# Optimization experiments

Hardware: AMD Instinct MI355X
Metric: run time of the kernel (lower is better)

## Reference

```python
import jax, jax.numpy as jnp
import numpy as np

T, B, D = 200, 1024, 128
T_OBS = 140
L = 20       # rec_dims: encoder latent per mean/std
LAT = 32     # latents: generative latent dim
GRU_U = 200  # gru_units
UNITS = 100  # hidden units of ODE-func / z0 nets


def _lin(key, fan_in, fan_out):
    return jax.random.normal(key, (fan_in, fan_out), jnp.float32) / jnp.sqrt(jnp.float32(fan_in))


def setup_inputs() -> dict:
    key = jax.random.key(0)
    ks = jax.random.split(key, 20)
    gin = 2 * L + 2 * D  # GRU input: (mean,std) + (data,mask)
    inp = {
        "truth": jax.random.normal(ks[0], (T, B, D), jnp.float32),
        "t": jnp.arange(T, dtype=jnp.float32),
        "obs_idx": jnp.sort(jax.random.randint(ks[1], (T_OBS,), 0, T)),
        "eps": jax.random.normal(ks[2], (B, LAT), jnp.float32),
        # encoder ODE func (rec_layers=1 hidden layer of UNITS)
        "enc_w1": _lin(ks[3], L, UNITS), "enc_b1": jnp.zeros(UNITS, jnp.float32),
        "enc_w2": _lin(ks[4], UNITS, L), "enc_b2": jnp.zeros(L, jnp.float32),
        # GRU unit: update / reset / new-state nets
        "gru_uw1": _lin(ks[5], gin, GRU_U), "gru_ub1": jnp.zeros(GRU_U, jnp.float32),
        "gru_uw2": _lin(ks[6], GRU_U, 2 * L), "gru_ub2": jnp.zeros(2 * L, jnp.float32),
        "gru_rw1": _lin(ks[7], gin, GRU_U), "gru_rb1": jnp.zeros(GRU_U, jnp.float32),
        "gru_rw2": _lin(ks[8], GRU_U, 2 * L), "gru_rb2": jnp.zeros(2 * L, jnp.float32),
        "gru_nw1": _lin(ks[9], gin, GRU_U), "gru_nb1": jnp.zeros(GRU_U, jnp.float32),
        "gru_nw2": _lin(ks[10], GRU_U, 2 * L), "gru_nb2": jnp.zeros(2 * L, jnp.float32),
        # transform hidden -> z0 (mean,std)
        "z0_w1": _lin(ks[11], 2 * L, UNITS), "z0_b1": jnp.zeros(UNITS, jnp.float32),
        "z0_w2": _lin(ks[12], UNITS, 2 * LAT), "z0_b2": jnp.zeros(2 * LAT, jnp.float32),
        # decoder ODE func (gen_layers=2 hidden layers of UNITS)
        "dec_w1": _lin(ks[13], LAT, UNITS), "dec_b1": jnp.zeros(UNITS, jnp.float32),
        "dec_w2": _lin(ks[14], UNITS, UNITS), "dec_b2": jnp.zeros(UNITS, jnp.float32),
        "dec_w3": _lin(ks[15], UNITS, LAT), "dec_b3": jnp.zeros(LAT, jnp.float32),
        # readout latent -> data space
        "out_w": _lin(ks[16], LAT, D), "out_b": jnp.zeros(D, jnp.float32),
    }
    return inp


def _rk4(f, y, dt):
    k1 = f(y)
    k2 = f(y + 0.5 * dt * k1)
    k3 = f(y + 0.5 * dt * k2)
    k4 = f(y + dt * k3)
    return y + (dt / 6.0) * (k1 + 2.0 * k2 + 2.0 * k3 + k4)


def reference(truth, t, obs_idx, eps,
              enc_w1, enc_b1, enc_w2, enc_b2,
              gru_uw1, gru_ub1, gru_uw2, gru_ub2,
              gru_rw1, gru_rb1, gru_rw2, gru_rb2,
              gru_nw1, gru_nb1, gru_nw2, gru_nb2,
              z0_w1, z0_b1, z0_w2, z0_b2,
              dec_w1, dec_b1, dec_w2, dec_b2, dec_w3, dec_b3,
              out_w, out_b):
    enc_f = lambda y: jnp.tanh(y @ enc_w1 + enc_b1) @ enc_w2 + enc_b2
    dec_f = lambda z: (jnp.tanh(jnp.tanh(z @ dec_w1 + dec_b1) @ dec_w2 + dec_b2)
                       @ dec_w3 + dec_b3)

    # ----- ODE-RNN encoder, run_backwards=True over observed timesteps -----
    x_obs = truth[obs_idx][::-1]                     # [To, B, D], time-reversed
    t_obs = t[obs_idx][::-1]
    dts = jnp.concatenate([jnp.zeros(1, t.dtype), jnp.diff(t_obs)])  # <=0 steps

    def enc_step(carry, inp):
        ym, ys = carry                               # [B,L] each
        x, dt = inp
        ym = _rk4(enc_f, ym, dt)                     # evolve mean between obs
        xm = jnp.concatenate([x, jnp.ones_like(x)], -1)   # data + mask(=1)
        y = jnp.concatenate([ym, ys], -1)            # [B, 2L]
        yc = jnp.concatenate([y, xm], -1)            # [B, 2L+2D]
        u = jax.nn.sigmoid(jnp.tanh(yc @ gru_uw1 + gru_ub1) @ gru_uw2 + gru_ub2)
        r = jax.nn.sigmoid(jnp.tanh(yc @ gru_rw1 + gru_rb1) @ gru_rw2 + gru_rb2)
        nc = jnp.concatenate([y * r, xm], -1)
        ns = jnp.tanh(nc @ gru_nw1 + gru_nb1) @ gru_nw2 + gru_nb2
        nm, nsd = ns[:, :L], jnp.abs(ns[:, L:])
        new_y = (1.0 - u) * jnp.concatenate([nm, nsd], -1) + u * y
        return (new_y[:, :L], new_y[:, L:]), None

    nb = truth.shape[1]
    init = (jnp.zeros((nb, L), truth.dtype), jnp.zeros((nb, L), truth.dtype))
    (ym, ys), _ = jax.lax.scan(enc_step, init, (x_obs, dts))

    # ----- z0 posterior and sample (n_traj_samples=1) -----
    h = jnp.tanh(jnp.concatenate([ym, ys], -1) @ z0_w1 + z0_b1) @ z0_w2 + z0_b2
    z0_mean, z0_std = h[:, :LAT], jnp.abs(h[:, LAT:])
    z = z0_mean + eps * z0_std                       # [B, LAT]

    # ----- Neural ODE decoder over time_steps_to_predict = t -----
    def dec_step(zc, dt):
        zn = _rk4(dec_f, zc, dt)
        return zn, zn
    _, zs = jax.lax.scan(dec_step, z, jnp.diff(t))
    sol = jnp.concatenate([z[None], zs], 0)          # [T, B, LAT]

    out = sol @ out_w + out_b                        # [T, B, D]
    return jnp.transpose(out, (1, 0, 2))[None]       # [1, B, T, D]
```

## Files before the change

kernel.cpp:

```cpp
#include <hip/hip_runtime.h>
#include <math.h>

#define BB 1024
#define DD 128
#define NWG 256
#define CH 28
#define NCH 5

#define WS_WPACK 0
#define WS_B1E   81920
#define WS_W1Y   82560
#define WS_Y     106560
#define WS_Z     147520
#define WS_HPRE  180288
#define WS_SOL   180288

__device__ __forceinline__ float bcast(float v, int lane) {
    return __uint_as_float(__builtin_amdgcn_readlane(__float_as_uint(v), lane));
}

__device__ __forceinline__ float tanh_fast(float x) {
    const float t = __builtin_amdgcn_exp2f(x * 2.88539008177793f);
    return 1.f - 2.f * __builtin_amdgcn_rcpf(t + 1.f);
}

__global__ __launch_bounds__(256) void prep_kernel(
    const float* __restrict__ uw1, const float* __restrict__ ub1,
    const float* __restrict__ rw1, const float* __restrict__ rb1,
    const float* __restrict__ nw1, const float* __restrict__ nb1,
    float* __restrict__ ws)
{
    int tid = blockIdx.x * blockDim.x + threadIdx.x;
    int nth = gridDim.x * blockDim.x;
    for (int idx = tid; idx < 128 * 640; idx += nth) {
        int k = idx / 640, j = idx - k * 640;
        float v = 0.f;
        if (j < 600) {
            int g = j / 200, jj = j - g * 200;
            const float* w1 = (g == 0) ? uw1 : (g == 1) ? rw1 : nw1;
            v = w1[(40 + k) * 200 + jj];
        }
        ws[WS_WPACK + idx] = v;
    }
    for (int j = tid; j < 640; j += nth) {
        float s = 0.f;
        if (j < 600) {
            int g = j / 200, jj = j - g * 200;
            const float* w1 = (g == 0) ? uw1 : (g == 1) ? rw1 : nw1;
            const float* b1 = (g == 0) ? ub1 : (g == 1) ? rb1 : nb1;
            s = b1[jj];
            for (int k = 168; k < 296; ++k) s += w1[k * 200 + jj];
        }
        ws[WS_B1E + j] = s;
    }
    for (int idx = tid; idx < 40 * 600; idx += nth) {
        int k = idx / 600, j = idx - k * 600;
        int g = j / 200, jj = j - g * 200;
        const float* w1 = (g == 0) ? uw1 : (g == 1) ? rw1 : nw1;
        ws[WS_W1Y + idx] = w1[k * 200 + jj];
    }
}

__global__ __launch_bounds__(256) void hpre_gemm(
    const float* __restrict__ truth, const int* __restrict__ obs_idx,
    const float* __restrict__ ws, float* __restrict__ hpre, int s0)
{
    __shared__ float sx[64][68];
    __shared__ float sw[64][132];
    const int t0 = threadIdx.x;
    const int jt = blockIdx.x % 5;
    const int bt = (blockIdx.x / 5) % 16;
    const int sl = blockIdx.x / 80;
    const int oi = obs_idx[139 - (s0 + sl)];
    const int b0 = bt * 64;
    const float* wpack = ws + WS_WPACK;
    const float* b1e   = ws + WS_B1E;

    const int jj  = t0 & 15;
    const int bb4 = t0 >> 4;
    float acc[8][4];
#pragma unroll
    for (int m = 0; m < 8; ++m)
#pragma unroll
        for (int q = 0; q < 4; ++q) acc[m][q] = 0.f;

    for (int kh = 0; kh < 2; ++kh) {
        __syncthreads();
        for (int i = t0; i < 64 * 16; i += 256) {
            int bb = i >> 4, kq = i & 15;
            const float4 v = *(const float4*)&truth[((size_t)oi * BB + b0 + bb) * DD + kh * 64 + kq * 4];
            *(float4*)&sx[bb][kq * 4] = v;
        }
        for (int i = t0; i < 64 * 32; i += 256) {
            int kk = i >> 5, jq = i & 31;
            const float4 v = *(const float4*)&wpack[(kh * 64 + kk) * 640 + jt * 128 + jq * 4];
            *(float4*)&sw[kk][jq * 4] = v;
        }
        __syncthreads();
#pragma unroll 4
        for (int k = 0; k < 64; ++k) {
            float xv[4], wv[8];
#pragma unroll
            for (int q = 0; q < 4; ++q) xv[q] = sx[bb4 * 4 + q][k];
#pragma unroll
            for (int m = 0; m < 8; ++m) wv[m] = sw[k][jj + 16 * m];
#pragma unroll
            for (int m = 0; m < 8; ++m)
#pragma unroll
                for (int q = 0; q < 4; ++q) acc[m][q] += wv[m] * xv[q];
        }
    }
    const int bblk = bt * 16 + bb4;
#pragma unroll
    for (int m = 0; m < 8; ++m) {
        int j = jt * 128 + jj + 16 * m;
        if (j < 600) {
            float be = b1e[j];
#pragma unroll
            for (int q = 0; q < 4; ++q)
                hpre[(size_t)((sl * 256 + bblk) * 4 + q) * 600 + j] = acc[m][q] + be;
        }
    }
}

__global__ __launch_bounds__(256, 1) void enc_chunk(
    const float* __restrict__ tg, const int* __restrict__ obs_idx,
    const float* __restrict__ eps,
    const float* __restrict__ ew1, const float* __restrict__ eb1,
    const float* __restrict__ ew2, const float* __restrict__ eb2,
    const float* __restrict__ uw2, const float* __restrict__ ub2,
    const float* __restrict__ rw2, const float* __restrict__ rb2,
    const float* __restrict__ nw2, const float* __restrict__ nb2,
    const float* __restrict__ z0w1, const float* __restrict__ z0b1,
    const float* __restrict__ z0w2, const float* __restrict__ z0b2,
    float* __restrict__ ws, int s0)
{
    __shared__ float s_t[200];
    __shared__ int   s_oi[140];
    __shared__ __align__(16) float s_y[40][4];
    __shared__ __align__(16) float s_ytmp[20][4];
    __shared__ float s_kacc[20][4];
    __shared__ __align__(16) float s_hid[4][104];
    __shared__ float s_pe[20][4][2];
    __shared__ __align__(16) float s_ew1t[100 * 20];
    __shared__ __align__(16) float s_w2n[40 * 212];
    __shared__ __align__(16) float s_hur[4][416];
    __shared__ __align__(16) float s_hn[4][208];
    __shared__ float s_pw[80][4][4];
    __shared__ float s_pn[40][4][4];
    __shared__ float s_u[40][4];
    __shared__ __align__(16) float s_yr[40][4];
    __shared__ float s_z0o[4][64];

    const int t0 = threadIdx.x;
    const int bblk = blockIdx.x;
    const int b0 = bblk * 4;
    const float* hpre = ws + WS_HPRE;

    float rgy[3][40];
    float rew2h[52];
    float rw2q[2][52];
    float eb1_r = 0.f, eb2_r = 0.f, bur_r = 0.f, bn_r = 0.f;

    if (t0 < 200) {
#pragma unroll
        for (int g = 0; g < 3; ++g)
#pragma unroll
            for (int k = 0; k < 40; ++k)
                rgy[g][k] = ws[WS_W1Y + k * 600 + g * 200 + t0];
    }
    if (t0 < 100) eb1_r = eb1[t0];
    if (t0 < 160) {
        const int c2 = t0 % 20, kh = t0 / 80;
#pragma unroll
        for (int i = 0; i < 52; ++i) {
            const int row = kh * 52 + i;
            rew2h[i] = (row < 100) ? ew2[row * 20 + c2] : 0.f;
        }
    }
    if (t0 < 80) eb2_r = eb2[t0 % 20];
    if (t0 < 160) {
        const int p = t0 % 20, g = (t0 / 20) % 2, kq = t0 / 40;
        const float* w2 = g ? rw2 : uw2;
#pragma unroll
        for (int j = 0; j < 2; ++j)
#pragma unroll
            for (int i = 0; i < 52; ++i) {
                const int row = kq * 52 + i;
                rw2q[j][i] = (row < 200) ? w2[row * 40 + p + 20 * j] : 0.f;
            }
        bur_r = ((t0 % 80) < 40) ? ub2[t0 % 80] : rb2[(t0 % 80) - 40];
        bn_r = nb2[t0 % 40];
    }

    for (int i = t0; i < 2000; i += 256) { int k = i / 100, c = i % 100; s_ew1t[c * 20 + k] = ew1[i]; }
    for (int i = t0; i < 40 * 212; i += 256) { int o = i / 212, k = i % 212; s_w2n[i] = (k < 200) ? nw2[k * 40 + o] : 0.f; }
    for (int i = t0; i < 200; i += 256) s_t[i] = tg[i];
    for (int i = t0; i < 140; i += 256) s_oi[i] = obs_idx[i];
    if (t0 < 160) { int k = t0 % 40, b = t0 / 40; s_y[k][b] = s0 ? ws[WS_Y + k * 1024 + b0 + b] : 0.f; }
    if (t0 < 4) {
#pragma unroll
        for (int i = 0; i < 4; ++i) s_hid[t0][100 + i] = 0.f;
#pragma unroll
        for (int i = 0; i < 8; ++i) { s_hur[t0][200 + i] = 0.f; s_hur[t0][408 + i] = 0.f; s_hn[t0][200 + i] = 0.f; }
    }
    __syncthreads();

    for (int sl = 0; sl < CH; ++sl) {
        const int s = s0 + sl;
        const int oi = s_oi[139 - s];
        const float dt = (s == 0) ? 0.f : (s_t[oi] - s_t[s_oi[140 - s]]);

        float hpu[4], hpr[4], hpn[4];
        if (t0 < 200) {
#pragma unroll
            for (int q = 0; q < 4; ++q) {
                const size_t r = (size_t)((sl * 256 + bblk) * 4 + q) * 600;
                hpu[q] = hpre[r + t0];
                hpr[q] = hpre[r + 200 + t0];
                hpn[q] = hpre[r + 400 + t0];
            }
        }

#pragma unroll 1
        for (int e = 0; e < 4; ++e) {
            if (t0 < 100) {
                const int c = t0;
                float a[4] = {eb1_r, eb1_r, eb1_r, eb1_r};
#pragma unroll
                for (int i = 0; i < 5; ++i) {
                    const float4 wv = *(const float4*)&s_ew1t[c * 20 + 4 * i];
                    const float wk[4] = {wv.x, wv.y, wv.z, wv.w};
#pragma unroll
                    for (int kk = 0; kk < 4; ++kk) {
                        const int k = 4 * i + kk;
                        const float4 yv = (e == 0) ? *(const float4*)&s_y[k][0]
                                                   : *(const float4*)&s_ytmp[k][0];
                        a[0] += wk[kk] * yv.x; a[1] += wk[kk] * yv.y;
                        a[2] += wk[kk] * yv.z; a[3] += wk[kk] * yv.w;
                    }
                }
#pragma unroll
                for (int b = 0; b < 4; ++b) s_hid[b][c] = tanhf(a[b]);
            }
            __syncthreads();
            if (t0 < 160) {
                const int c2 = t0 % 20, b = (t0 / 20) % 4, kh = t0 / 80;
                float acc = 0.f;
#pragma unroll
                for (int i = 0; i < 13; ++i) {
                    const float4 hv = *(const float4*)&s_hid[b][kh * 52 + 4 * i];
                    acc += hv.x * rew2h[4 * i] + hv.y * rew2h[4 * i + 1]
                         + hv.z * rew2h[4 * i + 2] + hv.w * rew2h[4 * i + 3];
                }
                s_pe[c2][b][kh] = acc;
            }
            __syncthreads();
            if (t0 < 80) {
                const int c2 = t0 % 20, b = t0 / 20;
                const float kv = eb2_r + s_pe[c2][b][0] + s_pe[c2][b][1];
                const float y0 = s_y[c2][b];
                if (e == 0)      { s_kacc[c2][b] = kv;        s_ytmp[c2][b] = y0 + 0.5f * dt * kv; }
                else if (e == 1) { s_kacc[c2][b] += 2.f * kv; s_ytmp[c2][b] = y0 + 0.5f * dt * kv; }
                else if (e == 2) { s_kacc[c2][b] += 2.f * kv; s_ytmp[c2][b] = y0 + dt * kv; }
                else             { s_y[c2][b] = y0 + (dt / 6.f) * (s_kacc[c2][b] + kv); }
            }
            __syncthreads();
        }

        if (t0 < 200) {
            float au[4], ar[4];
#pragma unroll
            for (int b = 0; b < 4; ++b) { au[b] = hpu[b]; ar[b] = hpr[b]; }
#pragma unroll
            for (int k = 0; k < 40; ++k) {
                const float4 yv = *(const float4*)&s_y[k][0];
                const float wu = rgy[0][k], wr = rgy[1][k];
                au[0] += wu * yv.x; au[1] += wu * yv.y; au[2] += wu * yv.z; au[3] += wu * yv.w;
                ar[0] += wr * yv.x; ar[1] += wr * yv.y; ar[2] += wr * yv.z; ar[3] += wr * yv.w;
            }
#pragma unroll
            for (int b = 0; b < 4; ++b) {
                s_hur[b][t0] = tanhf(au[b]);
                s_hur[b][208 + t0] = tanhf(ar[b]);
            }
        }
        __syncthreads();

        if (t0 < 160) {
            const int p = t0 % 20, g = (t0 / 20) % 2, kq = t0 / 40;
            const int goff = g * 208;
            float a1[4] = {0.f, 0.f, 0.f, 0.f}, a2[4] = {0.f, 0.f, 0.f, 0.f};
#pragma unroll
            for (int i = 0; i < 13; ++i) {
                const float wa = rw2q[0][4 * i], wb = rw2q[0][4 * i + 1],
                            wc = rw2q[0][4 * i + 2], wd = rw2q[0][4 * i + 3];
                const float we = rw2q[1][4 * i], wf = rw2q[1][4 * i + 1],
                            wg = rw2q[1][4 * i + 2], wh = rw2q[1][4 * i + 3];
#pragma unroll
                for (int b = 0; b < 4; ++b) {
                    const float4 hv = *(const float4*)&s_hur[b][goff + kq * 52 + 4 * i];
                    a1[b] += hv.x * wa + hv.y * wb + hv.z * wc + hv.w * wd;
                    a2[b] += hv.x * we + hv.y * wf + hv.z * wg + hv.w * wh;
                }
            }
            const int o1 = 40 * g + p, o2 = o1 + 20;
#pragma unroll
            for (int b = 0; b < 4; ++b) { s_pw[o1][b][kq] = a1[b]; s_pw[o2][b][kq] = a2[b]; }
        }
        __syncthreads();

        if (t0 < 160) {
            const int o = t0 % 80, bp = t0 / 80;
#pragma unroll
            for (int j = 0; j < 2; ++j) {
                const int b = 2 * bp + j;
                const float v = bur_r + s_pw[o][b][0] + s_pw[o][b][1] + s_pw[o][b][2] + s_pw[o][b][3];
                const float sg = 1.f / (1.f + expf(-v));
                if (o < 40) s_u[o][b] = sg;
                else        s_yr[o - 40][b] = s_y[o - 40][b] * sg;
            }
        }
        __syncthreads();

        if (t0 < 200) {
            float an[4];
#pragma unroll
            for (int b = 0; b < 4; ++b) an[b] = hpn[b];
#pragma unroll
            for (int k = 0; k < 40; ++k) {
                const float4 yv = *(const float4*)&s_yr[k][0];
                const float w = rgy[2][k];
                an[0] += w * yv.x; an[1] += w * yv.y; an[2] += w * yv.z; an[3] += w * yv.w;
            }
#pragma unroll
            for (int b = 0; b < 4; ++b) s_hn[b][t0] = tanhf(an[b]);
        }
        __syncthreads();

        if (t0 < 160) {
            const int o = t0 % 40, kq = t0 / 40;
            float an[4] = {0.f, 0.f, 0.f, 0.f};
#pragma unroll
            for (int i = 0; i < 13; ++i) {
                const float4 wv = *(const float4*)&s_w2n[o * 212 + kq * 52 + 4 * i];
#pragma unroll
                for (int b = 0; b < 4; ++b) {
                    const float4 hv = *(const float4*)&s_hn[b][kq * 52 + 4 * i];
                    an[b] += hv.x * wv.x + hv.y * wv.y + hv.z * wv.z + hv.w * wv.w;
                }
            }
#pragma unroll
            for (int b = 0; b < 4; ++b) s_pn[o][b][kq] = an[b];
        }
        __syncthreads();

        if (t0 < 160) {
            const int o = t0 % 40, b = t0 / 40;
            const float v = bn_r + s_pn[o][b][0] + s_pn[o][b][1] + s_pn[o][b][2] + s_pn[o][b][3];
            const float cand = (o < 20) ? v : fabsf(v);
            const float uu = s_u[o][b];
            s_y[o][b] = (1.f - uu) * cand + uu * s_y[o][b];
        }
        __syncthreads();
    }

    if (s0 + CH == 140) {
        if (t0 < 100) {
            const int c = t0;
            float a[4] = {z0b1[c], z0b1[c], z0b1[c], z0b1[c]};
#pragma unroll
            for (int k = 0; k < 40; ++k) {
                const float4 yv = *(const float4*)&s_y[k][0];
                const float w = z0w1[k * 100 + c];
                a[0] += w * yv.x; a[1] += w * yv.y; a[2] += w * yv.z; a[3] += w * yv.w;
            }
#pragma unroll
            for (int b = 0; b < 4; ++b) s_hid[b][c] = tanhf(a[b]);
        }
        __syncthreads();
        {
            const int b = t0 / 64, u = t0 % 64;
            float acc = z0b2[u];
#pragma unroll
            for (int i = 0; i < 25; ++i) {
                const float4 hv = *(const float4*)&s_hid[b][4 * i];
                acc += hv.x * z0w2[(4 * i) * 64 + u] + hv.y * z0w2[(4 * i + 1) * 64 + u]
                     + hv.z * z0w2[(4 * i + 2) * 64 + u] + hv.w * z0w2[(4 * i + 3) * 64 + u];
            }
            s_z0o[b][u] = acc;
        }
        __syncthreads();
        if (t0 < 128) {
            const int b = t0 / 32, i = t0 % 32;
            const int gb = b0 + b;
            ws[WS_Z + gb * 32 + i] = s_z0o[b][i] + eps[gb * 32 + i] * fabsf(s_z0o[b][32 + i]);
        }
    }
    if (t0 < 160) {
        const int k = t0 % 40, b = t0 / 40;
        ws[WS_Y + k * 1024 + b0 + b] = s_y[k][b];
    }
}

__global__ __launch_bounds__(128, 2) void dec_kernel(
    const float* __restrict__ tg,
    const float* __restrict__ dw1, const float* __restrict__ db1,
    const float* __restrict__ dw2, const float* __restrict__ db2,
    const float* __restrict__ dw3, const float* __restrict__ db3,
    float* __restrict__ ws)
{
    __shared__ float s_t[200];
    __shared__ float s_p1[2][100];
    __shared__ float s_p2[2][100];
    __shared__ float s_p3[2][32];

    const int t0 = threadIdx.x;
    const int w  = t0 >> 6;
    const int l  = t0 & 63;
    const int batch = blockIdx.x;

    const int c0 = l;
    const int c1 = 64 + l;
    const bool has1 = (l < 36);
    const int j3 = l & 31;

    float rw1a[16], rw1b[16], rw2a[50], rw2b[50], rw3[50];
#pragma unroll
    for (int i = 0; i < 16; ++i) {
        rw1a[i] = dw1[(16 * w + i) * 100 + c0];
        rw1b[i] = has1 ? dw1[(16 * w + i) * 100 + c1] : 0.f;
    }
#pragma unroll
    for (int i = 0; i < 50; ++i) {
        rw2a[i] = dw2[(50 * w + i) * 100 + c0];
        rw2b[i] = has1 ? dw2[(50 * w + i) * 100 + c1] : 0.f;
        rw3[i]  = dw3[(50 * w + i) * 32 + j3];
    }
    const float rb1a = db1[c0];
    const float rb1b = has1 ? db1[c1] : 0.f;
    const float rb2a = db2[c0];
    const float rb2b = has1 ? db2[c1] : 0.f;
    const float rb3  = db3[j3];

    for (int i = t0; i < 200; i += 128) s_t[i] = tg[i];

    float z_r = ws[WS_Z + (size_t)batch * 32 + j3];
    __syncthreads();

    float zs = z_r, ka_r = 0.f;

    for (int s = 0; s < 200; ++s) {
        if (t0 < 32)
            ws[WS_SOL + (size_t)(s * 1024 + batch) * 32 + l] = z_r;
        if (s == 199) break;
        const float dtv = s_t[s + 1] - s_t[s];

#pragma unroll 1
        for (int e = 0; e < 4; ++e) {
            float a0 = 0.f, a1 = 0.f;
            if (w == 0) {
#pragma unroll
                for (int i = 0; i < 16; ++i) {
                    const float sv = bcast(zs, i);
                    a0 += sv * rw1a[i]; a1 += sv * rw1b[i];
                }
            } else {
#pragma unroll
                for (int i = 0; i < 16; ++i) {
                    const float sv = bcast(zs, 16 + i);
                    a0 += sv * rw1a[i]; a1 += sv * rw1b[i];
                }
            }
            s_p1[w][c0] = a0;
            if (has1) s_p1[w][c1] = a1;
            __syncthreads();
            const float h1_0 = tanh_fast(rb1a + a0 + s_p1[w ^ 1][c0]);
            const float h1_1 = has1 ? tanh_fast(rb1b + a1 + s_p1[w ^ 1][c1]) : 0.f;

            float a2 = 0.f, a3 = 0.f;
            if (w == 0) {
#pragma unroll
                for (int i = 0; i < 50; ++i) {
                    const float sv = bcast(h1_0, i);
                    a2 += sv * rw2a[i]; a3 += sv * rw2b[i];
                }
            } else {
#pragma unroll
                for (int i = 0; i < 14; ++i) {
                    const float sv = bcast(h1_0, 50 + i);
                    a2 += sv * rw2a[i]; a3 += sv * rw2b[i];
                }
#pragma unroll
                for (int i = 14; i < 50; ++i) {
                    const float sv = bcast(h1_1, i - 14);
                    a2 += sv * rw2a[i]; a3 += sv * rw2b[i];
                }
            }
            s_p2[w][c0] = a2;
            if (has1) s_p2[w][c1] = a3;
            __syncthreads();
            const float h2_0 = tanh_fast(rb2a + a2 + s_p2[w ^ 1][c0]);
            const float h2_1 = has1 ? tanh_fast(rb2b + a3 + s_p2[w ^ 1][c1]) : 0.f;

            float ap = 0.f;
            if (w == 0) {
#pragma unroll
                for (int i = 0; i < 50; ++i) ap += bcast(h2_0, i) * rw3[i];
            } else {
#pragma unroll
                for (int i = 0; i < 14; ++i) ap += bcast(h2_0, 50 + i) * rw3[i];
#pragma unroll
                for (int i = 14; i < 50; ++i) ap += bcast(h2_1, i - 14) * rw3[i];
            }
            if (l < 32) s_p3[w][l] = ap;
            __syncthreads();
            const float kj = rb3 + s_p3[0][j3] + s_p3[1][j3];

            if (e == 0)      { ka_r = kj;        zs = z_r + 0.5f * dtv * kj; }
            else if (e == 1) { ka_r += 2.f * kj; zs = z_r + 0.5f * dtv * kj; }
            else if (e == 2) { ka_r += 2.f * kj; zs = z_r + dtv * kj; }
            else             { z_r += (dtv / 6.f) * (ka_r + kj); zs = z_r; }
        }
    }
}

__global__ __launch_bounds__(256) void proj_kernel(
    const float* __restrict__ ow, const float* __restrict__ ob,
    const float* __restrict__ ws, float* __restrict__ out)
{
    const int t0 = threadIdx.x;
    const int d = t0 & 127, half = t0 >> 7;
    float rw[32];
#pragma unroll
    for (int k = 0; k < 32; ++k) rw[k] = ow[k * 128 + d];
    const float bo = ob[d];
    const int sb0 = blockIdx.x * 64 + half * 32;
#pragma unroll 2
    for (int m = 0; m < 32; ++m) {
        const int sb = sb0 + m;
        const int s = sb >> 10, b = sb & 1023;
        const float4* zp = (const float4*)&ws[WS_SOL + (size_t)sb * 32];
        float acc = bo;
#pragma unroll
        for (int kq = 0; kq < 8; ++kq) {
            const float4 zv = zp[kq];
            acc += zv.x * rw[4 * kq] + zv.y * rw[4 * kq + 1]
                 + zv.z * rw[4 * kq + 2] + zv.w * rw[4 * kq + 3];
        }
        out[((size_t)b * 200 + s) * 128 + d] = acc;
    }
}

extern "C" void kernel_launch(void* const* d_in, const int* in_sizes, int n_in,
                              void* d_out, int out_size, void* d_ws, size_t ws_size,
                              hipStream_t stream)
{
    const float* truth = (const float*)d_in[0];
    const float* tg    = (const float*)d_in[1];
    const int*   oi    = (const int*)d_in[2];
    const float* eps   = (const float*)d_in[3];
    const float* ew1   = (const float*)d_in[4];
    const float* eb1   = (const float*)d_in[5];
    const float* ew2   = (const float*)d_in[6];
    const float* eb2   = (const float*)d_in[7];
    const float* uw1   = (const float*)d_in[8];
    const float* ub1   = (const float*)d_in[9];
    const float* uw2   = (const float*)d_in[10];
    const float* ub2   = (const float*)d_in[11];
    const float* rw1   = (const float*)d_in[12];
    const float* rb1   = (const float*)d_in[13];
    const float* rw2   = (const float*)d_in[14];
    const float* rb2   = (const float*)d_in[15];
    const float* nw1   = (const float*)d_in[16];
    const float* nb1   = (const float*)d_in[17];
    const float* nw2   = (const float*)d_in[18];
    const float* nb2   = (const float*)d_in[19];
    const float* z0w1  = (const float*)d_in[20];
    const float* z0b1  = (const float*)d_in[21];
    const float* z0w2  = (const float*)d_in[22];
    const float* z0b2  = (const float*)d_in[23];
    const float* dw1   = (const float*)d_in[24];
    const float* db1   = (const float*)d_in[25];
    const float* dw2   = (const float*)d_in[26];
    const float* db2   = (const float*)d_in[27];
    const float* dw3   = (const float*)d_in[28];
    const float* db3   = (const float*)d_in[29];
    const float* ow    = (const float*)d_in[30];
    const float* ob    = (const float*)d_in[31];
    float* ws  = (float*)d_ws;
    float* out = (float*)d_out;

    prep_kernel<<<dim3(120), dim3(256), 0, stream>>>(uw1, ub1, rw1, rb1, nw1, nb1, ws);
    for (int c = 0; c < NCH; ++c) {
        hpre_gemm<<<dim3(CH * 16 * 5), dim3(256), 0, stream>>>(truth, oi, ws, ws + WS_HPRE, c * CH);
        enc_chunk<<<dim3(NWG), dim3(256), 0, stream>>>(
            tg, oi, eps, ew1, eb1, ew2, eb2, uw2, ub2, rw2, rb2, nw2, nb2,
            z0w1, z0b1, z0w2, z0b2, ws, c * CH);
    }
    dec_kernel<<<dim3(1024), dim3(128), 0, stream>>>(tg, dw1, db1, dw2, db2, dw3, db3, ws);
    proj_kernel<<<dim3(3200), dim3(256), 0, stream>>>(ow, ob, ws, out);
}
```

Measured before the change: 4.102 ms.

## Split decoder ODE MLP across four waves with LDS-broadcast activations

```diff
diff --git a/kernel.cpp b/kernel.cpp
--- a/kernel.cpp
+++ b/kernel.cpp
@@ -14,10 +14,6 @@
 #define WS_Z     147520
 #define WS_HPRE  180288
 #define WS_SOL   180288
-
-__device__ __forceinline__ float bcast(float v, int lane) {
-    return __uint_as_float(__builtin_amdgcn_readlane(__float_as_uint(v), lane));
-}
 
 __device__ __forceinline__ float tanh_fast(float x) {
     const float t = __builtin_amdgcn_exp2f(x * 2.88539008177793f);
@@ -403,7 +399,7 @@
     }
 }
 
-__global__ __launch_bounds__(128, 2) void dec_kernel(
+__global__ __launch_bounds__(256, 3) void dec_kernel(
     const float* __restrict__ tg,
     const float* __restrict__ dw1, const float* __restrict__ db1,
     const float* __restrict__ dw2, const float* __restrict__ db2,
@@ -411,13 +407,17 @@
     float* __restrict__ ws)
 {
     __shared__ float s_t[200];
-    __shared__ float s_p1[2][100];
-    __shared__ float s_p2[2][100];
-    __shared__ float s_p3[2][32];
+    __shared__ __align__(16) float s_z[32];
+    __shared__ __align__(16) float s_h1[112];
+    __shared__ __align__(16) float s_h2[112];
+    __shared__ float s_p1[4][100];
+    __shared__ float s_p2[4][100];
+    __shared__ float s_p3[8][32];
 
     const int t0 = threadIdx.x;
     const int w  = t0 >> 6;
     const int l  = t0 & 63;
+    const int hk = l >> 5;
     const int batch = blockIdx.x;
 
     const int c0 = l;
@@ -425,102 +425,98 @@
     const bool has1 = (l < 36);
     const int j3 = l & 31;
 
-    float rw1a[16], rw1b[16], rw2a[50], rw2b[50], rw3[50];
-#pragma unroll
-    for (int i = 0; i < 16; ++i) {
-        rw1a[i] = dw1[(16 * w + i) * 100 + c0];
-        rw1b[i] = has1 ? dw1[(16 * w + i) * 100 + c1] : 0.f;
-    }
-#pragma unroll
-    for (int i = 0; i < 50; ++i) {
-        rw2a[i] = dw2[(50 * w + i) * 100 + c0];
-        rw2b[i] = has1 ? dw2[(50 * w + i) * 100 + c1] : 0.f;
-        rw3[i]  = dw3[(50 * w + i) * 32 + j3];
-    }
-    const float rb1a = db1[c0];
-    const float rb1b = has1 ? db1[c1] : 0.f;
-    const float rb2a = db2[c0];
-    const float rb2b = has1 ? db2[c1] : 0.f;
-    const float rb3  = db3[j3];
-
-    for (int i = t0; i < 200; i += 128) s_t[i] = tg[i];
-
-    float z_r = ws[WS_Z + (size_t)batch * 32 + j3];
+    float rw1a[8], rw1b[8], rw2a[28], rw2b[28], rw3[14];
+#pragma unroll
+    for (int i = 0; i < 8; ++i) {
+        rw1a[i] = dw1[(8 * w + i) * 100 + c0];
+        rw1b[i] = has1 ? dw1[(8 * w + i) * 100 + c1] : 0.f;
+    }
+#pragma unroll
+    for (int i = 0; i < 28; ++i) {
+        const int row = 28 * w + i;
+        const bool v = (row < 100);
+        rw2a[i] = v ? dw2[row * 100 + c0] : 0.f;
+        rw2b[i] = (v && has1) ? dw2[row * 100 + c1] : 0.f;
+    }
+#pragma unroll
+    for (int i = 0; i < 14; ++i) {
+        const int row = 28 * w + 14 * hk + i;
+        rw3[i] = (row < 100) ? dw3[row * 32 + j3] : 0.f;
+    }
+    float b1_r = 0.f, b2_r = 0.f, b3_r = 0.f;
+    if (t0 < 100) { b1_r = db1[t0]; b2_r = db2[t0]; }
+    if (t0 < 32)  b3_r = db3[t0];
+
+    for (int i = t0; i < 200; i += 256) s_t[i] = tg[i];
+    if (t0 >= 100 && t0 < 112) { s_h1[t0] = 0.f; s_h2[t0] = 0.f; }
+
+    float z_r = 0.f, ka_r = 0.f;
+    if (t0 < 32) { z_r = ws[WS_Z + (size_t)batch * 32 + t0]; s_z[t0] = z_r; }
     __syncthreads();
-
-    float zs = z_r, ka_r = 0.f;
 
     for (int s = 0; s < 200; ++s) {
         if (t0 < 32)
-            ws[WS_SOL + (size_t)(s * 1024 + batch) * 32 + l] = z_r;
+            ws[WS_SOL + (size_t)(s * 1024 + batch) * 32 + t0] = z_r;
         if (s == 199) break;
         const float dtv = s_t[s + 1] - s_t[s];
 
 #pragma unroll 1
         for (int e = 0; e < 4; ++e) {
-            float a0 = 0.f, a1 = 0.f;
-            if (w == 0) {
-#pragma unroll
-                for (int i = 0; i < 16; ++i) {
-                    const float sv = bcast(zs, i);
-                    a0 += sv * rw1a[i]; a1 += sv * rw1b[i];
+            {
+                const float4 za = *(const float4*)&s_z[8 * w];
+                const float4 zb = *(const float4*)&s_z[8 * w + 4];
+                float a0 = za.x * rw1a[0] + za.y * rw1a[1] + za.z * rw1a[2] + za.w * rw1a[3]
+                         + zb.x * rw1a[4] + zb.y * rw1a[5] + zb.z * rw1a[6] + zb.w * rw1a[7];
+                float a1 = za.x * rw1b[0] + za.y * rw1b[1] + za.z * rw1b[2] + za.w * rw1b[3]
+                         + zb.x * rw1b[4] + zb.y * rw1b[5] + zb.z * rw1b[6] + zb.w * rw1b[7];
+                s_p1[w][c0] = a0;
+                if (has1) s_p1[w][c1] = a1;
+            }
+            __syncthreads();
+            if (t0 < 100)
+                s_h1[t0] = tanh_fast(b1_r + s_p1[0][t0] + s_p1[1][t0] + s_p1[2][t0] + s_p1[3][t0]);
+            __syncthreads();
+
+            {
+                float a2 = 0.f, a3 = 0.f;
+#pragma unroll
+                for (int i = 0; i < 7; ++i) {
+                    const float4 hv = *(const float4*)&s_h1[28 * w + 4 * i];
+                    a2 += hv.x * rw2a[4 * i] + hv.y * rw2a[4 * i + 1]
+                        + hv.z * rw2a[4 * i + 2] + hv.w * rw2a[4 * i + 3];
+                    a3 += hv.x * rw2b[4 * i] + hv.y * rw2b[4 * i + 1]
+                        + hv.z * rw2b[4 * i + 2] + hv.w * rw2b[4 * i + 3];
                 }
-            } else {
-#pragma unroll
-                for (int i = 0; i < 16; ++i) {
-                    const float sv = bcast(zs, 16 + i);
-                    a0 += sv * rw1a[i]; a1 += sv * rw1b[i];
+                s_p2[w][c0] = a2;
+                if (has1) s_p2[w][c1] = a3;
+            }
+            __syncthreads();
+            if (t0 < 100)
+                s_h2[t0] = tanh_fast(b2_r + s_p2[0][t0] + s_p2[1][t0] + s_p2[2][t0] + s_p2[3][t0]);
+            __syncthreads();
+
+            {
+                float ap = 0.f;
+#pragma unroll
+                for (int i = 0; i < 7; ++i) {
+                    const float2 hv = *(const float2*)&s_h2[28 * w + 14 * hk + 2 * i];
+                    ap += hv.x * rw3[2 * i] + hv.y * rw3[2 * i + 1];
                 }
-            }
-            s_p1[w][c0] = a0;
-            if (has1) s_p1[w][c1] = a1;
-            __syncthreads();
-            const float h1_0 = tanh_fast(rb1a + a0 + s_p1[w ^ 1][c0]);
-            const float h1_1 = has1 ? tanh_fast(rb1b + a1 + s_p1[w ^ 1][c1]) : 0.f;
-
-            float a2 = 0.f, a3 = 0.f;
-            if (w == 0) {
-#pragma unroll
-                for (int i = 0; i < 50; ++i) {
-                    const float sv = bcast(h1_0, i);
-                    a2 += sv * rw2a[i]; a3 += sv * rw2b[i];
-                }
-            } else {
-#pragma unroll
-                for (int i = 0; i < 14; ++i) {
-                    const float sv = bcast(h1_0, 50 + i);
-                    a2 += sv * rw2a[i]; a3 += sv * rw2b[i];
-                }
-#pragma unroll
-                for (int i = 14; i < 50; ++i) {
-                    const float sv = bcast(h1_1, i - 14);
-                    a2 += sv * rw2a[i]; a3 += sv * rw2b[i];
-                }
-            }
-            s_p2[w][c0] = a2;
-            if (has1) s_p2[w][c1] = a3;
-            __syncthreads();
-            const float h2_0 = tanh_fast(rb2a + a2 + s_p2[w ^ 1][c0]);
-            const float h2_1 = has1 ? tanh_fast(rb2b + a3 + s_p2[w ^ 1][c1]) : 0.f;
-
-            float ap = 0.f;
-            if (w == 0) {
-#pragma unroll
-                for (int i = 0; i < 50; ++i) ap += bcast(h2_0, i) * rw3[i];
-            } else {
-#pragma unroll
-                for (int i = 0; i < 14; ++i) ap += bcast(h2_0, 50 + i) * rw3[i];
-#pragma unroll
-                for (int i = 14; i < 50; ++i) ap += bcast(h2_1, i - 14) * rw3[i];
-            }
-            if (l < 32) s_p3[w][l] = ap;
-            __syncthreads();
-            const float kj = rb3 + s_p3[0][j3] + s_p3[1][j3];
-
-            if (e == 0)      { ka_r = kj;        zs = z_r + 0.5f * dtv * kj; }
-            else if (e == 1) { ka_r += 2.f * kj; zs = z_r + 0.5f * dtv * kj; }
-            else if (e == 2) { ka_r += 2.f * kj; zs = z_r + dtv * kj; }
-            else             { z_r += (dtv / 6.f) * (ka_r + kj); zs = z_r; }
+                s_p3[2 * w + hk][j3] = ap;
+            }
+            __syncthreads();
+            if (t0 < 32) {
+                const float kj = b3_r
+                    + s_p3[0][t0] + s_p3[1][t0] + s_p3[2][t0] + s_p3[3][t0]
+                    + s_p3[4][t0] + s_p3[5][t0] + s_p3[6][t0] + s_p3[7][t0];
+                float zs;
+                if (e == 0)      { ka_r = kj;        zs = z_r + 0.5f * dtv * kj; }
+                else if (e == 1) { ka_r += 2.f * kj; zs = z_r + 0.5f * dtv * kj; }
+                else if (e == 2) { ka_r += 2.f * kj; zs = z_r + dtv * kj; }
+                else             { z_r += (dtv / 6.f) * (ka_r + kj); zs = z_r; }
+                s_z[t0] = zs;
+            }
+            __syncthreads();
         }
     }
 }
@@ -598,6 +594,6 @@
             tg, oi, eps, ew1, eb1, ew2, eb2, uw2, ub2, rw2, rb2, nw2, nb2,
             z0w1, z0b1, z0w2, z0b2, ws, c * CH);
     }
-    dec_kernel<<<dim3(1024), dim3(128), 0, stream>>>(tg, dw1, db1, dw2, db2, dw3, db3, ws);
+    dec_kernel<<<dim3(1024), dim3(256), 0, stream>>>(tg, dw1, db1, dw2, db2, dw3, db3, ws);
     proj_kernel<<<dim3(3200), dim3(256), 0, stream>>>(ow, ob, ws, out);
 }
```

Result: slower. 4.514 ms (+10.0%).

## Split decoder ODE reduction across three wavefronts and use fast tanh/sigmoid in encoder

Applied to the files above, without the earlier changes.

```diff
diff --git a/kernel.cpp b/kernel.cpp
--- a/kernel.cpp
+++ b/kernel.cpp
@@ -22,6 +22,10 @@
 __device__ __forceinline__ float tanh_fast(float x) {
     const float t = __builtin_amdgcn_exp2f(x * 2.88539008177793f);
     return 1.f - 2.f * __builtin_amdgcn_rcpf(t + 1.f);
+}
+__device__ __forceinline__ float sigm_fast(float x) {
+    const float t = __builtin_amdgcn_exp2f(x * -1.4426950408889634f);
+    return __builtin_amdgcn_rcpf(1.f + t);
 }
 
 __global__ __launch_bounds__(256) void prep_kernel(
@@ -241,7 +245,7 @@
                     }
                 }
 #pragma unroll
-                for (int b = 0; b < 4; ++b) s_hid[b][c] = tanhf(a[b]);
+                for (int b = 0; b < 4; ++b) s_hid[b][c] = tanh_fast(a[b]);
             }
             __syncthreads();
             if (t0 < 160) {
@@ -281,8 +285,8 @@
             }
 #pragma unroll
             for (int b = 0; b < 4; ++b) {
-                s_hur[b][t0] = tanhf(au[b]);
-                s_hur[b][208 + t0] = tanhf(ar[b]);
+                s_hur[b][t0] = tanh_fast(au[b]);
+                s_hur[b][208 + t0] = tanh_fast(ar[b]);
             }
         }
         __syncthreads();
@@ -316,7 +320,7 @@
             for (int j = 0; j < 2; ++j) {
                 const int b = 2 * bp + j;
                 const float v = bur_r + s_pw[o][b][0] + s_pw[o][b][1] + s_pw[o][b][2] + s_pw[o][b][3];
-                const float sg = 1.f / (1.f + expf(-v));
+                const float sg = sigm_fast(v);
                 if (o < 40) s_u[o][b] = sg;
                 else        s_yr[o - 40][b] = s_y[o - 40][b] * sg;
             }
@@ -334,7 +338,7 @@
                 an[0] += w * yv.x; an[1] += w * yv.y; an[2] += w * yv.z; an[3] += w * yv.w;
             }
 #pragma unroll
-            for (int b = 0; b < 4; ++b) s_hn[b][t0] = tanhf(an[b]);
+            for (int b = 0; b < 4; ++b) s_hn[b][t0] = tanh_fast(an[b]);
         }
         __syncthreads();
 
@@ -376,7 +380,7 @@
                 a[0] += w * yv.x; a[1] += w * yv.y; a[2] += w * yv.z; a[3] += w * yv.w;
             }
 #pragma unroll
-            for (int b = 0; b < 4; ++b) s_hid[b][c] = tanhf(a[b]);
+            for (int b = 0; b < 4; ++b) s_hid[b][c] = tanh_fast(a[b]);
         }
         __syncthreads();
         {
@@ -403,7 +407,7 @@
     }
 }
 
-__global__ __launch_bounds__(128, 2) void dec_kernel(
+__global__ __launch_bounds__(192, 2) void dec_kernel(
     const float* __restrict__ tg,
     const float* __restrict__ dw1, const float* __restrict__ db1,
     const float* __restrict__ dw2, const float* __restrict__ db2,
@@ -411,12 +415,12 @@
     float* __restrict__ ws)
 {
     __shared__ float s_t[200];
-    __shared__ float s_p1[2][100];
-    __shared__ float s_p2[2][100];
-    __shared__ float s_p3[2][32];
+    __shared__ float s_p1[3][100];
+    __shared__ float s_p2[3][100];
+    __shared__ float s_p3[3][32];
 
     const int t0 = threadIdx.x;
-    const int w  = t0 >> 6;
+    const int w  = t0 / 64;
     const int l  = t0 & 63;
     const int batch = blockIdx.x;
 
@@ -424,105 +428,140 @@
     const int c1 = 64 + l;
     const bool has1 = (l < 36);
     const int j3 = l & 31;
-
-    float rw1a[16], rw1b[16], rw2a[50], rw2b[50], rw3[50];
-#pragma unroll
-    for (int i = 0; i < 16; ++i) {
-        rw1a[i] = dw1[(16 * w + i) * 100 + c0];
-        rw1b[i] = has1 ? dw1[(16 * w + i) * 100 + c1] : 0.f;
-    }
-#pragma unroll
-    for (int i = 0; i < 50; ++i) {
-        rw2a[i] = dw2[(50 * w + i) * 100 + c0];
-        rw2b[i] = has1 ? dw2[(50 * w + i) * 100 + c1] : 0.f;
-        rw3[i]  = dw3[(50 * w + i) * 32 + j3];
+    const int w1i = (w == 2) ? 0 : w + 1;
+    const int w2i = (w1i == 2) ? 0 : w1i + 1;
+
+    const int r1 = (w == 0) ? 0 : (w == 1) ? 11 : 22;
+    const int n1 = (w == 2) ? 10 : 11;
+    const int r2 = (w == 0) ? 0 : (w == 1) ? 34 : 67;
+    const int n2 = (w == 0) ? 34 : 33;
+
+    float rw1a[11], rw1b[11], rw2a[34], rw2b[34], rw3[34];
+#pragma unroll
+    for (int i = 0; i < 11; ++i) {
+        const bool v = (i < n1);
+        rw1a[i] = v ? dw1[(r1 + i) * 100 + c0] : 0.f;
+        rw1b[i] = (v && has1) ? dw1[(r1 + i) * 100 + c1] : 0.f;
+    }
+#pragma unroll
+    for (int i = 0; i < 34; ++i) {
+        const bool v = (i < n2);
+        rw2a[i] = v ? dw2[(r2 + i) * 100 + c0] : 0.f;
+        rw2b[i] = (v && has1) ? dw2[(r2 + i) * 100 + c1] : 0.f;
+        rw3[i]  = v ? dw3[(r2 + i) * 32 + j3] : 0.f;
     }
     const float rb1a = db1[c0];
     const float rb1b = has1 ? db1[c1] : 0.f;
     const float rb2a = db2[c0];
     const float rb2b = has1 ? db2[c1] : 0.f;
-    const float rb3  = db3[j3];
-
-    for (int i = t0; i < 200; i += 128) s_t[i] = tg[i];
+    const float b3d  = db3[j3];
+
+    for (int i = t0; i < 200; i += 192) s_t[i] = tg[i];
 
     float z_r = ws[WS_Z + (size_t)batch * 32 + j3];
+    float ka_r = 0.f;
+    float zs = z_r;
     __syncthreads();
-
-    float zs = z_r, ka_r = 0.f;
 
     for (int s = 0; s < 200; ++s) {
         if (t0 < 32)
-            ws[WS_SOL + (size_t)(s * 1024 + batch) * 32 + l] = z_r;
+            ws[WS_SOL + (size_t)(s * 1024 + batch) * 32 + t0] = z_r;
         if (s == 199) break;
         const float dtv = s_t[s + 1] - s_t[s];
 
 #pragma unroll 1
         for (int e = 0; e < 4; ++e) {
-            float a0 = 0.f, a1 = 0.f;
-            if (w == 0) {
-#pragma unroll
-                for (int i = 0; i < 16; ++i) {
-                    const float sv = bcast(zs, i);
-                    a0 += sv * rw1a[i]; a1 += sv * rw1b[i];
+            {
+                float a0 = 0.f, a1 = 0.f;
+                if (w == 0) {
+#pragma unroll
+                    for (int i = 0; i < 11; ++i) {
+                        const float sv = bcast(zs, i);
+                        a0 += sv * rw1a[i]; a1 += sv * rw1b[i];
+                    }
+                } else if (w == 1) {
+#pragma unroll
+                    for (int i = 0; i < 11; ++i) {
+                        const float sv = bcast(zs, 11 + i);
+                        a0 += sv * rw1a[i]; a1 += sv * rw1b[i];
+                    }
+                } else {
+#pragma unroll
+                    for (int i = 0; i < 10; ++i) {
+                        const float sv = bcast(zs, 22 + i);
+                        a0 += sv * rw1a[i]; a1 += sv * rw1b[i];
+                    }
                 }
-            } else {
-#pragma unroll
-                for (int i = 0; i < 16; ++i) {
-                    const float sv = bcast(zs, 16 + i);
-                    a0 += sv * rw1a[i]; a1 += sv * rw1b[i];
+                s_p1[w][c0] = a0;
+                if (has1) s_p1[w][c1] = a1;
+            }
+            __syncthreads();
+
+            const float h1_0 = tanh_fast(rb1a + s_p1[0][c0] + s_p1[1][c0] + s_p1[2][c0]);
+            const float h1_1 = has1 ? tanh_fast(rb1b + s_p1[0][c1] + s_p1[1][c1] + s_p1[2][c1]) : 0.f;
+
+            {
+                float a2 = 0.f, a3 = 0.f;
+                if (w == 0) {
+#pragma unroll
+                    for (int i = 0; i < 34; ++i) {
+                        const float sv = bcast(h1_0, i);
+                        a2 += sv * rw2a[i]; a3 += sv * rw2b[i];
+                    }
+                } else if (w == 1) {
+#pragma unroll
+                    for (int i = 0; i < 30; ++i) {
+                        const float sv = bcast(h1_0, 34 + i);
+                        a2 += sv * rw2a[i]; a3 += sv * rw2b[i];
+                    }
+#pragma unroll
+                    for (int i = 30; i < 33; ++i) {
+                        const float sv = bcast(h1_1, i - 30);
+                        a2 += sv * rw2a[i]; a3 += sv * rw2b[i];
+                    }
+                } else {
+#pragma unroll
+                    for (int i = 0; i < 33; ++i) {
+                        const float sv = bcast(h1_1, 3 + i);
+                        a2 += sv * rw2a[i]; a3 += sv * rw2b[i];
+                    }
                 }
-            }
-            s_p1[w][c0] = a0;
-            if (has1) s_p1[w][c1] = a1;
+                s_p2[w][c0] = a2;
+                if (has1) s_p2[w][c1] = a3;
+            }
             __syncthreads();
-            const float h1_0 = tanh_fast(rb1a + a0 + s_p1[w ^ 1][c0]);
-            const float h1_1 = has1 ? tanh_fast(rb1b + a1 + s_p1[w ^ 1][c1]) : 0.f;
-
-            float a2 = 0.f, a3 = 0.f;
-            if (w == 0) {
-#pragma unroll
-                for (int i = 0; i < 50; ++i) {
-                    const float sv = bcast(h1_0, i);
-                    a2 += sv * rw2a[i]; a3 += sv * rw2b[i];
+
+            const float h2_0 = tanh_fast(rb2a + s_p2[0][c0] + s_p2[1][c0] + s_p2[2][c0]);
+            const float h2_1 = has1 ? tanh_fast(rb2b + s_p2[0][c1] + s_p2[1][c1] + s_p2[2][c1]) : 0.f;
+
+            {
+                float ap = 0.f;
+                if (w == 0) {
+#pragma unroll
+                    for (int i = 0; i < 34; ++i) ap += bcast(h2_0, i) * rw3[i];
+                } else if (w == 1) {
+#pragma unroll
+                    for (int i = 0; i < 30; ++i) ap += bcast(h2_0, 34 + i) * rw3[i];
+#pragma unroll
+                    for (int i = 30; i < 33; ++i) ap += bcast(h2_1, i - 30) * rw3[i];
+                } else {
+#pragma unroll
+                    for (int i = 0; i < 33; ++i) ap += bcast(h2_1, 3 + i) * rw3[i];
                 }
-            } else {
-#pragma unroll
-                for (int i = 0; i < 14; ++i) {
-                    const float sv = bcast(h1_0, 50 + i);
-                    a2 += sv * rw2a[i]; a3 += sv * rw2b[i];
-                }
-#pragma unroll
-                for (int i = 14; i < 50; ++i) {
-                    const float sv = bcast(h1_1, i - 14);
-                    a2 += sv * rw2a[i]; a3 += sv * rw2b[i];
-                }
-            }
-            s_p2[w][c0] = a2;
-            if (has1) s_p2[w][c1] = a3;
+                if (l < 32) s_p3[w][l] = ap;
+            }
             __syncthreads();
-            const float h2_0 = tanh_fast(rb2a + a2 + s_p2[w ^ 1][c0]);
-            const float h2_1 = has1 ? tanh_fast(rb2b + a3 + s_p2[w ^ 1][c1]) : 0.f;
-
-            float ap = 0.f;
-            if (w == 0) {
-#pragma unroll
-                for (int i = 0; i < 50; ++i) ap += bcast(h2_0, i) * rw3[i];
-            } else {
-#pragma unroll
-                for (int i = 0; i < 14; ++i) ap += bcast(h2_0, 50 + i) * rw3[i];
-#pragma unroll
-                for (int i = 14; i < 50; ++i) ap += bcast(h2_1, i - 14) * rw3[i];
-            }
-            if (l < 32) s_p3[w][l] = ap;
-            __syncthreads();
-            const float kj = rb3 + s_p3[0][j3] + s_p3[1][j3];
-
-            if (e == 0)      { ka_r = kj;        zs = z_r + 0.5f * dtv * kj; }
-            else if (e == 1) { ka_r += 2.f * kj; zs = z_r + 0.5f * dtv * kj; }
-            else if (e == 2) { ka_r += 2.f * kj; zs = z_r + dtv * kj; }
-            else             { z_r += (dtv / 6.f) * (ka_r + kj); zs = z_r; }
-        }
-    }
+
+            {
+                const float kj = b3d + s_p3[0][j3] + s_p3[1][j3] + s_p3[2][j3];
+                if (e == 0)      { ka_r = kj;        zs = z_r + 0.5f * dtv * kj; }
+                else if (e == 1) { ka_r += 2.f * kj; zs = z_r + 0.5f * dtv * kj; }
+                else if (e == 2) { ka_r += 2.f * kj; zs = z_r + dtv * kj; }
+                else             { z_r += (dtv / 6.f) * (ka_r + kj); zs = z_r; }
+            }
+        }
+    }
+    (void)w1i; (void)w2i;
 }
 
 __global__ __launch_bounds__(256) void proj_kernel(
@@ -598,6 +637,6 @@
             tg, oi, eps, ew1, eb1, ew2, eb2, uw2, ub2, rw2, rb2, nw2, nb2,
             z0w1, z0b1, z0w2, z0b2, ws, c * CH);
     }
-    dec_kernel<<<dim3(1024), dim3(128), 0, stream>>>(tg, dw1, db1, dw2, db2, dw3, db3, ws);
+    dec_kernel<<<dim3(1024), dim3(192), 0, stream>>>(tg, dw1, db1, dw2, db2, dw3, db3, ws);
     proj_kernel<<<dim3(3200), dim3(256), 0, stream>>>(ow, ob, ws, out);
 }
```

New measurement: 4.404 ms. 7.4% more time.
